# Performance work log

Hardware: AMD Instinct MI355X
Metric: run time of the kernel (lower is better)

The kernel has to match this reference:

```python
import jax, jax.numpy as jnp
import numpy as np

N = 50000
E = 600000
D_IN, D_HID, D_OUT = 128, 128, 64


def gcn_conv(x, edge_index, W, b):
    """PyG GCNConv: add self-loops, symmetric deg^{-1/2} normalization,
    linear transform, scatter-add aggregation, bias."""
    n = x.shape[0]
    loop = jnp.arange(n, dtype=edge_index.dtype)
    src = jnp.concatenate([edge_index[0], loop])
    dst = jnp.concatenate([edge_index[1], loop])
    h = x @ W  # [N, out]
    deg = jax.ops.segment_sum(jnp.ones_like(dst, dtype=h.dtype), dst, num_segments=n)
    dinv = jnp.where(deg > 0, jax.lax.rsqrt(jnp.maximum(deg, 1e-12)), 0.0)
    norm = dinv[src] * dinv[dst]  # [E+N]
    msg = h[src] * norm[:, None]  # gather + scale
    out = jax.ops.segment_sum(msg, dst, num_segments=n)  # scatter-add
    return out + b


def setup_inputs() -> dict:
    key = jax.random.key(0)
    k1, k2, k3, k4 = jax.random.split(key, 4)
    x = jax.random.normal(k1, (N, D_IN), dtype=jnp.float32)
    edge_index = jax.random.randint(k2, (2, E), 0, N, dtype=jnp.int64)
    s1 = (1.0 / np.sqrt(D_IN)).astype(np.float32) if False else np.float32(1.0 / np.sqrt(D_IN))
    s2 = np.float32(1.0 / np.sqrt(D_HID))
    W1 = jax.random.normal(k3, (D_IN, D_HID), dtype=jnp.float32) * s1
    b1 = jnp.zeros((D_HID,), dtype=jnp.float32)
    W2 = jax.random.normal(k4, (D_HID, D_OUT), dtype=jnp.float32) * s2
    b2 = jnp.zeros((D_OUT,), dtype=jnp.float32)
    return {"x": x, "edge_index": edge_index, "W1": W1, "b1": b1, "W2": W2, "b2": b2}


def reference(x, edge_index, W1, b1, W2, b2):
    # eval mode: dropout p = 0
    h = jax.nn.relu(gcn_conv(x, edge_index, W1, b1))
    return gcn_conv(h, edge_index, W2, b2)
```

## Files before the change

### kernel.cpp

```cpp
#include <hip/hip_runtime.h>
#include <hip/hip_fp16.h>
#include <stdint.h>

#define DIN 128
#define DHID 128
#define DOUT2 64

typedef __attribute__((ext_vector_type(8))) short short8v;
typedef __attribute__((ext_vector_type(4))) float f32x4;

__device__ __forceinline__ unsigned short f2bf(float f) {
    unsigned u = __float_as_uint(f);
    u += 0x7fffu + ((u >> 16) & 1u);
    return (unsigned short)(u >> 16);
}
__device__ __forceinline__ float bf2f(unsigned short b) {
    return __uint_as_float(((unsigned)b) << 16);
}
__device__ __forceinline__ float bflo(unsigned v) { return __uint_as_float(v << 16); }
__device__ __forceinline__ float bfhi(unsigned v) { return __uint_as_float(v & 0xffff0000u); }
__device__ __forceinline__ unsigned short f2h(float f) {
    return __half_as_ushort(__float2half_rn(f));
}
__device__ __forceinline__ float h2f(unsigned bits) {
    return __half2float(__ushort_as_half((unsigned short)bits));
}

__global__ void detect_i64_kernel(const unsigned* ei, int* flag) {
    int t = threadIdx.x;
    unsigned hi = ei[2 * t + 1];
    unsigned long long vote = __ballot(hi == 0u);
    if (t == 0) *flag = (vote == ~0ull) ? 1 : 0;
}

__global__ void deg_count_kernel(const int* ei32, const long long* ei64, const int* flag,
                                 unsigned* deg, int E) {
    int e = blockIdx.x * blockDim.x + threadIdx.x;
    if (e >= E) return;
    int mode = *flag;
    int d = mode ? (int)ei64[(size_t)E + e] : ei32[(size_t)E + e];
    atomicAdd(&deg[d], 1u);
}

template <int DO, typename AT>
__global__ __launch_bounds__(256) void gemm_mfma_kernel(const AT* __restrict__ A,
                                                        const float* __restrict__ W,
                                                        unsigned short* __restrict__ out,
                                                        int M) {
    constexpr int NT = DO / 16;
    __shared__ unsigned short As[64 * 136];
    __shared__ unsigned short Wt[DO * 136];
    const int tid = threadIdx.x;
    const int row0 = blockIdx.x * 64;

    for (int idx = tid; idx < 128 * (DO / 4); idx += 256) {
        int k = idx / (DO / 4);
        int n4 = (idx % (DO / 4)) * 4;
        float4 w = ((const float4*)W)[idx];
        Wt[(n4 + 0) * 136 + k] = f2bf(w.x);
        Wt[(n4 + 1) * 136 + k] = f2bf(w.y);
        Wt[(n4 + 2) * 136 + k] = f2bf(w.z);
        Wt[(n4 + 3) * 136 + k] = f2bf(w.w);
    }
    if constexpr (sizeof(AT) == 4) {
        for (int idx = tid; idx < 64 * 32; idx += 256) {
            int r = idx >> 5, c4 = idx & 31;
            int row = row0 + r;
            ushort4 o = {0, 0, 0, 0};
            if (row < M) {
                float4 v = ((const float4*)A)[(size_t)row * 32 + c4];
                o.x = f2bf(v.x);
                o.y = f2bf(v.y);
                o.z = f2bf(v.z);
                o.w = f2bf(v.w);
            }
            *(ushort4*)&As[r * 136 + c4 * 4] = o;
        }
    } else {
        for (int idx = tid; idx < 64 * 16; idx += 256) {
            int r = idx >> 4, c8 = idx & 15;
            int row = row0 + r;
            uint4 v = {0u, 0u, 0u, 0u};
            if (row < M) v = ((const uint4*)A)[(size_t)row * 16 + c8];
            *(uint4*)&As[r * 136 + c8 * 8] = v;
        }
    }
    __syncthreads();

    const int wid = tid >> 6, lane = tid & 63;
    const int r16 = lane & 15, g = lane >> 4;
    f32x4 acc[NT];
#pragma unroll
    for (int n = 0; n < NT; n++) acc[n] = (f32x4){0.f, 0.f, 0.f, 0.f};

    const unsigned short* a_base = &As[(wid * 16 + r16) * 136 + g * 8];
    const unsigned short* b_base = &Wt[r16 * 136 + g * 8];
#pragma unroll
    for (int kk = 0; kk < 4; kk++) {
        short8v a = *(const short8v*)(a_base + kk * 32);
#pragma unroll
        for (int n = 0; n < NT; n++) {
            short8v b = *(const short8v*)(b_base + n * 16 * 136 + kk * 32);
            acc[n] = __builtin_amdgcn_mfma_f32_16x16x32_bf16(a, b, acc[n], 0, 0, 0);
        }
    }

    const int rbase = row0 + wid * 16 + g * 4;
#pragma unroll
    for (int n = 0; n < NT; n++) {
#pragma unroll
        for (int q = 0; q < 4; q++) {
            int row = rbase + q;
            if (row < M) out[(size_t)row * DO + n * 16 + r16] = f2bf(acc[n][q]);
        }
    }
}

__global__ __launch_bounds__(256) void scan_blocksum_kernel(const unsigned* deg, int* bsum,
                                                            float* dinv, int N) {
    __shared__ int s[256];
    int t = threadIdx.x;
    int base = blockIdx.x * 1024 + t * 4;
    int sum = 0;
    if (base + 3 < N) {
        int4 v = *(const int4*)((const int*)deg + base);
        sum = v.x + v.y + v.z + v.w;
        float4 dv;
        dv.x = rsqrtf((float)(v.x + 1));
        dv.y = rsqrtf((float)(v.y + 1));
        dv.z = rsqrtf((float)(v.z + 1));
        dv.w = rsqrtf((float)(v.w + 1));
        *(float4*)(dinv + base) = dv;
    } else {
        for (int j = 0; j < 4; j++)
            if (base + j < N) {
                int d = (int)deg[base + j];
                sum += d;
                dinv[base + j] = rsqrtf((float)(d + 1));
            }
    }
    s[t] = sum;
    __syncthreads();
    for (int off = 128; off > 0; off >>= 1) {
        if (t < off) s[t] += s[t + off];
        __syncthreads();
    }
    if (t == 0) bsum[blockIdx.x] = s[0];
}

__global__ __launch_bounds__(256) void scan_bsum_kernel(int* bsum, int* row_ptr, int nb, int N) {
    __shared__ int s[256];
    int t = threadIdx.x;
    int v = (t < nb) ? bsum[t] : 0;
    s[t] = v;
    __syncthreads();
    for (int off = 1; off < 256; off <<= 1) {
        int u = (t >= off) ? s[t - off] : 0;
        __syncthreads();
        s[t] += u;
        __syncthreads();
    }
    if (t < nb) bsum[t] = s[t] - v;
    if (t == 255) row_ptr[N] = s[255];
}

__global__ __launch_bounds__(256) void scan_write_kernel(const unsigned* deg, const int* bsum,
                                                         int* row_ptr, int* cursor, int N) {
    __shared__ int s[256];
    int t = threadIdx.x;
    int base = blockIdx.x * 1024 + t * 4;
    int d[4];
    int sum = 0;
#pragma unroll
    for (int j = 0; j < 4; j++) {
        int idx = base + j;
        d[j] = (idx < N) ? (int)deg[idx] : 0;
        sum += d[j];
    }
    s[t] = sum;
    __syncthreads();
    for (int off = 1; off < 256; off <<= 1) {
        int u = (t >= off) ? s[t - off] : 0;
        __syncthreads();
        s[t] += u;
        __syncthreads();
    }
    int run = bsum[blockIdx.x] + s[t] - sum;
#pragma unroll
    for (int j = 0; j < 4; j++) {
        int idx = base + j;
        if (idx < N) {
            row_ptr[idx] = run;
            cursor[idx] = run;
            run += d[j];
        }
    }
}

__global__ void scatter_pack32_kernel(const int* ei32, const long long* ei64, const int* flag,
                                      const float* dinv, int* cursor, unsigned* csr, int E) {
    int e = blockIdx.x * blockDim.x + threadIdx.x;
    if (e >= E) return;
    int mode = *flag;
    int s, d;
    if (mode) {
        s = (int)ei64[e];
        d = (int)ei64[(size_t)E + e];
    } else {
        s = ei32[e];
        d = ei32[(size_t)E + e];
    }
    int pos = atomicAdd(&cursor[d], 1);
    csr[pos] = (unsigned)s | ((unsigned)f2h(dinv[s]) << 16);
}

__global__ void scatter_pack64_kernel(const int* ei32, const long long* ei64, const int* flag,
                                      const float* dinv, int* cursor, unsigned long long* csr,
                                      int E) {
    int e = blockIdx.x * blockDim.x + threadIdx.x;
    if (e >= E) return;
    int mode = *flag;
    int s, d;
    if (mode) {
        s = (int)ei64[e];
        d = (int)ei64[(size_t)E + e];
    } else {
        s = ei32[e];
        d = ei32[(size_t)E + e];
    }
    int pos = atomicAdd(&cursor[d], 1);
    csr[pos] = (unsigned long long)(unsigned)s |
               ((unsigned long long)__float_as_uint(dinv[s]) << 32);
}

__device__ __forceinline__ void unpack(unsigned p, int& s, float& w) {
    s = (int)(p & 0xffffu);
    w = h2f(p >> 16);
}
__device__ __forceinline__ void unpack(unsigned long long p, int& s, float& w) {
    s = (int)(unsigned)(p & 0xffffffffu);
    w = __uint_as_float((unsigned)(p >> 32));
}

template <int D, bool RELU, typename OT, typename CT>
__global__ __launch_bounds__(256) void agg_kernel(const unsigned short* __restrict__ h,
                                                  const CT* __restrict__ csr,
                                                  const int* __restrict__ row_ptr,
                                                  const float* __restrict__ dinv,
                                                  const float* __restrict__ bias,
                                                  OT* __restrict__ out, int N) {
    const int wid = threadIdx.x >> 6;
    const int lane = threadIdx.x & 63;
    const int i = blockIdx.x * 4 + wid;
    if (i >= N) return;
    const float di = dinv[i];
    const int start = row_ptr[i], end = row_ptr[i + 1];

    if constexpr (D == 128) {
        const unsigned* hu = (const unsigned*)h;
        unsigned sv = hu[(size_t)i * 64 + lane];
        float a0 = di * bflo(sv), b0 = di * bfhi(sv);
        float a1 = 0.f, b1 = 0.f;
        int j = start;
        for (; j + 4 <= end; j += 4) {
            CT p0 = csr[j], p1 = csr[j + 1], p2 = csr[j + 2], p3 = csr[j + 3];
            int s0, s1, s2, s3;
            float w0, w1, w2, w3;
            unpack(p0, s0, w0);
            unpack(p1, s1, w1);
            unpack(p2, s2, w2);
            unpack(p3, s3, w3);
            unsigned v0 = hu[(size_t)s0 * 64 + lane];
            unsigned v1 = hu[(size_t)s1 * 64 + lane];
            unsigned v2 = hu[(size_t)s2 * 64 + lane];
            unsigned v3 = hu[(size_t)s3 * 64 + lane];
            a0 = fmaf(w0, bflo(v0), a0);
            b0 = fmaf(w0, bfhi(v0), b0);
            a1 = fmaf(w1, bflo(v1), a1);
            b1 = fmaf(w1, bfhi(v1), b1);
            a0 = fmaf(w2, bflo(v2), a0);
            b0 = fmaf(w2, bfhi(v2), b0);
            a1 = fmaf(w3, bflo(v3), a1);
            b1 = fmaf(w3, bfhi(v3), b1);
        }
        for (; j < end; ++j) {
            int s0;
            float w0;
            unpack(csr[j], s0, w0);
            unsigned v0 = hu[(size_t)s0 * 64 + lane];
            a0 = fmaf(w0, bflo(v0), a0);
            b0 = fmaf(w0, bfhi(v0), b0);
        }
        float2 bv = ((const float2*)bias)[lane];
        float rx = di * (a0 + a1) + bv.x;
        float ry = di * (b0 + b1) + bv.y;
        if (RELU) {
            rx = fmaxf(rx, 0.f);
            ry = fmaxf(ry, 0.f);
        }
        if constexpr (sizeof(OT) == 2) {
            unsigned pv = (unsigned)f2bf(rx) | ((unsigned)f2bf(ry) << 16);
            ((unsigned*)out)[(size_t)i * 64 + lane] = pv;
        } else {
            ((float2*)out)[(size_t)i * 64 + lane] = make_float2(rx, ry);
        }
    } else {
        float a0 = di * bf2f(h[(size_t)i * 64 + lane]);
        float a1 = 0.f;
        int j = start;
        for (; j + 4 <= end; j += 4) {
            CT p0 = csr[j], p1 = csr[j + 1], p2 = csr[j + 2], p3 = csr[j + 3];
            int s0, s1, s2, s3;
            float w0, w1, w2, w3;
            unpack(p0, s0, w0);
            unpack(p1, s1, w1);
            unpack(p2, s2, w2);
            unpack(p3, s3, w3);
            float v0 = bf2f(h[(size_t)s0 * 64 + lane]);
            float v1 = bf2f(h[(size_t)s1 * 64 + lane]);
            float v2 = bf2f(h[(size_t)s2 * 64 + lane]);
            float v3 = bf2f(h[(size_t)s3 * 64 + lane]);
            a0 = fmaf(w0, v0, a0);
            a1 = fmaf(w1, v1, a1);
            a0 = fmaf(w2, v2, a0);
            a1 = fmaf(w3, v3, a1);
        }
        for (; j < end; ++j) {
            int s0;
            float w0;
            unpack(csr[j], s0, w0);
            a0 = fmaf(w0, bf2f(h[(size_t)s0 * 64 + lane]), a0);
        }
        float r = di * (a0 + a1) + bias[lane];
        if (RELU) r = fmaxf(r, 0.f);
        if constexpr (sizeof(OT) == 2) {
            out[(size_t)i * 64 + lane] = (OT)f2bf(r);
        } else {
            out[(size_t)i * 64 + lane] = r;
        }
    }
}

extern "C" void kernel_launch(void* const* d_in, const int* in_sizes, int n_in,
                              void* d_out, int out_size, void* d_ws, size_t ws_size,
                              hipStream_t stream) {
    const float* x  = (const float*)d_in[0];
    const void*  ei = d_in[1];
    const float* W1 = (const float*)d_in[2];
    const float* b1 = (const float*)d_in[3];
    const float* W2 = (const float*)d_in[4];
    const float* b2 = (const float*)d_in[5];
    float* out = (float*)d_out;

    const int N = in_sizes[0] / DIN;
    const int E = in_sizes[1] / 2;

    char* ws = (char*)d_ws;
    size_t off = 0;
    auto alloc = [&](size_t bytes) -> void* {
        void* p = ws + off;
        off += (bytes + 255) & ~(size_t)255;
        return p;
    };
    unsigned*       deg  = (unsigned*)alloc((size_t)N * 4);
    float*          dinv = (float*)alloc((size_t)N * 4);
    int*            rowp = (int*)alloc((size_t)(N + 1) * 4);
    int*            curs = (int*)alloc((size_t)N * 4);
    int*            flag = (int*)alloc(256);
    int*            bsum = (int*)alloc(1024 * 4);
    void*           csr  = alloc((size_t)E * 8);
    unsigned short* h1   = (unsigned short*)alloc((size_t)N * DHID * 2);
    unsigned short* o1   = (unsigned short*)alloc((size_t)N * DHID * 2);
    unsigned short* h2   = h1;

    const int nb = (N + 1023) / 1024;
    const int gemmBlocks = (N + 63) / 64;
    const int degBlocks = (E + 255) / 256;

    hipMemsetAsync(deg, 0, (size_t)N * 4, stream);
    detect_i64_kernel<<<1, 64, 0, stream>>>((const unsigned*)ei, flag);
    deg_count_kernel<<<degBlocks, 256, 0, stream>>>((const int*)ei, (const long long*)ei, flag,
                                                    deg, E);
    gemm_mfma_kernel<DHID, float><<<gemmBlocks, 256, 0, stream>>>(x, W1, h1, N);
    scan_blocksum_kernel<<<nb, 256, 0, stream>>>(deg, bsum, dinv, N);
    scan_bsum_kernel<<<1, 256, 0, stream>>>(bsum, rowp, nb, N);
    scan_write_kernel<<<nb, 256, 0, stream>>>(deg, bsum, rowp, curs, N);

    if (N <= 65535) {
        unsigned* csr32 = (unsigned*)csr;
        scatter_pack32_kernel<<<degBlocks, 256, 0, stream>>>(
            (const int*)ei, (const long long*)ei, flag, dinv, curs, csr32, E);
        agg_kernel<DHID, true, unsigned short, unsigned><<<(N + 3) / 4, 256, 0, stream>>>(
            h1, csr32, rowp, dinv, b1, o1, N);
        gemm_mfma_kernel<DOUT2, unsigned short><<<gemmBlocks, 256, 0, stream>>>(o1, W2, h2, N);
        agg_kernel<DOUT2, false, float, unsigned><<<(N + 3) / 4, 256, 0, stream>>>(
            h2, csr32, rowp, dinv, b2, out, N);
    } else {
        unsigned long long* csr64 = (unsigned long long*)csr;
        scatter_pack64_kernel<<<degBlocks, 256, 0, stream>>>(
            (const int*)ei, (const long long*)ei, flag, dinv, curs, csr64, E);
        agg_kernel<DHID, true, unsigned short, unsigned long long><<<(N + 3) / 4, 256, 0,
                                                                     stream>>>(h1, csr64, rowp,
                                                                               dinv, b1, o1, N);
        gemm_mfma_kernel<DOUT2, unsigned short><<<gemmBlocks, 256, 0, stream>>>(o1, W2, h2, N);
        agg_kernel<DOUT2, false, float, unsigned long long><<<(N + 3) / 4, 256, 0, stream>>>(
            h2, csr64, rowp, dinv, b2, out, N);
    }
}
```

Before: 243.3 us.

## Pre-transpose weights once, fuse index-width detection into kernels, unroll aggregation by 8

A new prep kernel converts W1 and W2 to transposed bf16 once and also does the degree count with inline index-width detection. This removes the separate detect kernel, the flag memory read, and the per-block weight conversion in every GEMM block. The GEMM now reads B fragments straight from global or L2 instead of padded shared memory. The aggregation loops are unrolled to 8 edges with four accumulator pairs to keep more gathers in flight. The cost is that B loads now go through global memory rather than LDS, and register pressure in the aggregation kernel goes up.

```diff
diff --git a/kernel.cpp b/kernel.cpp
--- a/kernel.cpp
+++ b/kernel.cpp
@@ -26,42 +26,45 @@
     return __half2float(__ushort_as_half((unsigned short)bits));
 }
 
-__global__ void detect_i64_kernel(const unsigned* ei, int* flag) {
-    int t = threadIdx.x;
-    unsigned hi = ei[2 * t + 1];
-    unsigned long long vote = __ballot(hi == 0u);
-    if (t == 0) *flag = (vote == ~0ull) ? 1 : 0;
-}
-
-__global__ void deg_count_kernel(const int* ei32, const long long* ei64, const int* flag,
-                                 unsigned* deg, int E) {
-    int e = blockIdx.x * blockDim.x + threadIdx.x;
-    if (e >= E) return;
-    int mode = *flag;
-    int d = mode ? (int)ei64[(size_t)E + e] : ei32[(size_t)E + e];
-    atomicAdd(&deg[d], 1u);
+__device__ __forceinline__ int detect_mode(const unsigned* ei) {
+    int lane = threadIdx.x & 63;
+    unsigned hi = ei[2 * lane + 1];
+    return (__ballot(hi == 0u) == ~0ull) ? 1 : 0;
+}
+
+__global__ void prep_kernel(const float* __restrict__ W1, const float* __restrict__ W2,
+                            unsigned short* __restrict__ wt1, unsigned short* __restrict__ wt2,
+                            const int* ei32, const long long* ei64, unsigned* deg, int E) {
+    if (blockIdx.x == 0) {
+        for (int idx = threadIdx.x; idx < 128 * 128; idx += 256) {
+            int n = idx & 127, k = idx >> 7;
+            wt1[n * 128 + k] = f2bf(W1[idx]);
+        }
+    } else if (blockIdx.x == 1) {
+        for (int idx = threadIdx.x; idx < 128 * 64; idx += 256) {
+            int n = idx & 63, k = idx >> 6;
+            wt2[n * 128 + k] = f2bf(W2[idx]);
+        }
+    } else {
+        int mode = detect_mode((const unsigned*)ei32);
+        int e = (blockIdx.x - 2) * 256 + threadIdx.x;
+        if (e < E) {
+            int d = mode ? (int)ei64[(size_t)E + e] : ei32[(size_t)E + e];
+            atomicAdd(&deg[d], 1u);
+        }
+    }
 }
 
 template <int DO, typename AT>
 __global__ __launch_bounds__(256) void gemm_mfma_kernel(const AT* __restrict__ A,
-                                                        const float* __restrict__ W,
+                                                        const unsigned short* __restrict__ Wt,
                                                         unsigned short* __restrict__ out,
                                                         int M) {
     constexpr int NT = DO / 16;
     __shared__ unsigned short As[64 * 136];
-    __shared__ unsigned short Wt[DO * 136];
     const int tid = threadIdx.x;
     const int row0 = blockIdx.x * 64;
 
-    for (int idx = tid; idx < 128 * (DO / 4); idx += 256) {
-        int k = idx / (DO / 4);
-        int n4 = (idx % (DO / 4)) * 4;
-        float4 w = ((const float4*)W)[idx];
-        Wt[(n4 + 0) * 136 + k] = f2bf(w.x);
-        Wt[(n4 + 1) * 136 + k] = f2bf(w.y);
-        Wt[(n4 + 2) * 136 + k] = f2bf(w.z);
-        Wt[(n4 + 3) * 136 + k] = f2bf(w.w);
-    }
     if constexpr (sizeof(AT) == 4) {
         for (int idx = tid; idx < 64 * 32; idx += 256) {
             int r = idx >> 5, c4 = idx & 31;
@@ -94,13 +97,13 @@
     for (int n = 0; n < NT; n++) acc[n] = (f32x4){0.f, 0.f, 0.f, 0.f};
 
     const unsigned short* a_base = &As[(wid * 16 + r16) * 136 + g * 8];
-    const unsigned short* b_base = &Wt[r16 * 136 + g * 8];
+    const unsigned short* b_base = Wt + r16 * 128 + g * 8;
 #pragma unroll
     for (int kk = 0; kk < 4; kk++) {
         short8v a = *(const short8v*)(a_base + kk * 32);
 #pragma unroll
         for (int n = 0; n < NT; n++) {
-            short8v b = *(const short8v*)(b_base + n * 16 * 136 + kk * 32);
+            short8v b = *(const short8v*)(b_base + n * 16 * 128 + kk * 32);
             acc[n] = __builtin_amdgcn_mfma_f32_16x16x32_bf16(a, b, acc[n], 0, 0, 0);
         }
     }
@@ -197,11 +200,11 @@
     }
 }
 
-__global__ void scatter_pack32_kernel(const int* ei32, const long long* ei64, const int* flag,
-                                      const float* dinv, int* cursor, unsigned* csr, int E) {
+__global__ void scatter_pack32_kernel(const int* ei32, const long long* ei64, const float* dinv,
+                                      int* cursor, unsigned* csr, int E) {
+    int mode = detect_mode((const unsigned*)ei32);
     int e = blockIdx.x * blockDim.x + threadIdx.x;
     if (e >= E) return;
-    int mode = *flag;
     int s, d;
     if (mode) {
         s = (int)ei64[e];
@@ -214,12 +217,11 @@
     csr[pos] = (unsigned)s | ((unsigned)f2h(dinv[s]) << 16);
 }
 
-__global__ void scatter_pack64_kernel(const int* ei32, const long long* ei64, const int* flag,
-                                      const float* dinv, int* cursor, unsigned long long* csr,
-                                      int E) {
+__global__ void scatter_pack64_kernel(const int* ei32, const long long* ei64, const float* dinv,
+                                      int* cursor, unsigned long long* csr, int E) {
+    int mode = detect_mode((const unsigned*)ei32);
     int e = blockIdx.x * blockDim.x + threadIdx.x;
     if (e >= E) return;
-    int mode = *flag;
     int s, d;
     if (mode) {
         s = (int)ei64[e];
@@ -260,28 +262,32 @@
         const unsigned* hu = (const unsigned*)h;
         unsigned sv = hu[(size_t)i * 64 + lane];
         float a0 = di * bflo(sv), b0 = di * bfhi(sv);
-        float a1 = 0.f, b1 = 0.f;
+        float a1 = 0.f, b1 = 0.f, a2 = 0.f, b2 = 0.f, a3 = 0.f, b3 = 0.f;
         int j = start;
-        for (; j + 4 <= end; j += 4) {
-            CT p0 = csr[j], p1 = csr[j + 1], p2 = csr[j + 2], p3 = csr[j + 3];
-            int s0, s1, s2, s3;
-            float w0, w1, w2, w3;
-            unpack(p0, s0, w0);
-            unpack(p1, s1, w1);
-            unpack(p2, s2, w2);
-            unpack(p3, s3, w3);
-            unsigned v0 = hu[(size_t)s0 * 64 + lane];
-            unsigned v1 = hu[(size_t)s1 * 64 + lane];
-            unsigned v2 = hu[(size_t)s2 * 64 + lane];
-            unsigned v3 = hu[(size_t)s3 * 64 + lane];
-            a0 = fmaf(w0, bflo(v0), a0);
-            b0 = fmaf(w0, bfhi(v0), b0);
-            a1 = fmaf(w1, bflo(v1), a1);
-            b1 = fmaf(w1, bfhi(v1), b1);
-            a0 = fmaf(w2, bflo(v2), a0);
-            b0 = fmaf(w2, bfhi(v2), b0);
-            a1 = fmaf(w3, bflo(v3), a1);
-            b1 = fmaf(w3, bfhi(v3), b1);
+        for (; j + 8 <= end; j += 8) {
+            int s[8];
+            float w[8];
+            unsigned v[8];
+#pragma unroll
+            for (int u = 0; u < 8; u++) unpack(csr[j + u], s[u], w[u]);
+#pragma unroll
+            for (int u = 0; u < 8; u++) v[u] = hu[(size_t)s[u] * 64 + lane];
+            a0 = fmaf(w[0], bflo(v[0]), a0);
+            b0 = fmaf(w[0], bfhi(v[0]), b0);
+            a1 = fmaf(w[1], bflo(v[1]), a1);
+            b1 = fmaf(w[1], bfhi(v[1]), b1);
+            a2 = fmaf(w[2], bflo(v[2]), a2);
+            b2 = fmaf(w[2], bfhi(v[2]), b2);
+            a3 = fmaf(w[3], bflo(v[3]), a3);
+            b3 = fmaf(w[3], bfhi(v[3]), b3);
+            a0 = fmaf(w[4], bflo(v[4]), a0);
+            b0 = fmaf(w[4], bfhi(v[4]), b0);
+            a1 = fmaf(w[5], bflo(v[5]), a1);
+            b1 = fmaf(w[5], bfhi(v[5]), b1);
+            a2 = fmaf(w[6], bflo(v[6]), a2);
+            b2 = fmaf(w[6], bfhi(v[6]), b2);
+            a3 = fmaf(w[7], bflo(v[7]), a3);
+            b3 = fmaf(w[7], bfhi(v[7]), b3);
         }
         for (; j < end; ++j) {
             int s0;
@@ -292,8 +298,8 @@
             b0 = fmaf(w0, bfhi(v0), b0);
         }
         float2 bv = ((const float2*)bias)[lane];
-        float rx = di * (a0 + a1) + bv.x;
-        float ry = di * (b0 + b1) + bv.y;
+        float rx = di * ((a0 + a1) + (a2 + a3)) + bv.x;
+        float ry = di * ((b0 + b1) + (b2 + b3)) + bv.y;
         if (RELU) {
             rx = fmaxf(rx, 0.f);
             ry = fmaxf(ry, 0.f);
@@ -306,24 +312,24 @@
         }
     } else {
         float a0 = di * bf2f(h[(size_t)i * 64 + lane]);
-        float a1 = 0.f;
+        float a1 = 0.f, a2 = 0.f, a3 = 0.f;
         int j = start;
-        for (; j + 4 <= end; j += 4) {
-            CT p0 = csr[j], p1 = csr[j + 1], p2 = csr[j + 2], p3 = csr[j + 3];
-            int s0, s1, s2, s3;
-            float w0, w1, w2, w3;
-            unpack(p0, s0, w0);
-            unpack(p1, s1, w1);
-            unpack(p2, s2, w2);
-            unpack(p3, s3, w3);
-            float v0 = bf2f(h[(size_t)s0 * 64 + lane]);
-            float v1 = bf2f(h[(size_t)s1 * 64 + lane]);
-            float v2 = bf2f(h[(size_t)s2 * 64 + lane]);
-            float v3 = bf2f(h[(size_t)s3 * 64 + lane]);
-            a0 = fmaf(w0, v0, a0);
-            a1 = fmaf(w1, v1, a1);
-            a0 = fmaf(w2, v2, a0);
-            a1 = fmaf(w3, v3, a1);
+        for (; j + 8 <= end; j += 8) {
+            int s[8];
+            float w[8];
+            float v[8];
+#pragma unroll
+            for (int u = 0; u < 8; u++) unpack(csr[j + u], s[u], w[u]);
+#pragma unroll
+            for (int u = 0; u < 8; u++) v[u] = bf2f(h[(size_t)s[u] * 64 + lane]);
+            a0 = fmaf(w[0], v[0], a0);
+            a1 = fmaf(w[1], v[1], a1);
+            a2 = fmaf(w[2], v[2], a2);
+            a3 = fmaf(w[3], v[3], a3);
+            a0 = fmaf(w[4], v[4], a0);
+            a1 = fmaf(w[5], v[5], a1);
+            a2 = fmaf(w[6], v[6], a2);
+            a3 = fmaf(w[7], v[7], a3);
         }
         for (; j < end; ++j) {
             int s0;
@@ -331,7 +337,7 @@
             unpack(csr[j], s0, w0);
             a0 = fmaf(w0, bf2f(h[(size_t)s0 * 64 + lane]), a0);
         }
-        float r = di * (a0 + a1) + bias[lane];
+        float r = di * ((a0 + a1) + (a2 + a3)) + bias[lane];
         if (RELU) r = fmaxf(r, 0.f);
         if constexpr (sizeof(OT) == 2) {
             out[(size_t)i * 64 + lane] = (OT)f2bf(r);
@@ -366,8 +372,9 @@
     float*          dinv = (float*)alloc((size_t)N * 4);
     int*            rowp = (int*)alloc((size_t)(N + 1) * 4);
     int*            curs = (int*)alloc((size_t)N * 4);
-    int*            flag = (int*)alloc(256);
     int*            bsum = (int*)alloc(1024 * 4);
+    unsigned short* wt1  = (unsigned short*)alloc(128 * 128 * 2);
+    unsigned short* wt2  = (unsigned short*)alloc(128 * 64 * 2);
     void*           csr  = alloc((size_t)E * 8);
     unsigned short* h1   = (unsigned short*)alloc((size_t)N * DHID * 2);
     unsigned short* o1   = (unsigned short*)alloc((size_t)N * DHID * 2);
@@ -378,31 +385,32 @@
     const int degBlocks = (E + 255) / 256;
 
     hipMemsetAsync(deg, 0, (size_t)N * 4, stream);
-    detect_i64_kernel<<<1, 64, 0, stream>>>((const unsigned*)ei, flag);
-    deg_count_kernel<<<degBlocks, 256, 0, stream>>>((const int*)ei, (const long long*)ei, flag,
-                                                    deg, E);
-    gemm_mfma_kernel<DHID, float><<<gemmBlocks, 256, 0, stream>>>(x, W1, h1, N);
+    prep_kernel<<<2 + degBlocks, 256, 0, stream>>>(W1, W2, wt1, wt2, (const int*)ei,
+                                                   (const long long*)ei, deg, E);
+    gemm_mfma_kernel<DHID, float><<<gemmBlocks, 256, 0, stream>>>(x, wt1, h1, N);
     scan_blocksum_kernel<<<nb, 256, 0, stream>>>(deg, bsum, dinv, N);
     scan_bsum_kernel<<<1, 256, 0, stream>>>(bsum, rowp, nb, N);
     scan_write_kernel<<<nb, 256, 0, stream>>>(deg, bsum, rowp, curs, N);
 
     if (N <= 65535) {
         unsigned* csr32 = (unsigned*)csr;
-        scatter_pack32_kernel<<<degBlocks, 256, 0, stream>>>(
-            (const int*)ei, (const long long*)ei, flag, dinv, curs, csr32, E);
+        scatter_pack32_kernel<<<degBlocks, 256, 0, stream>>>((const int*)ei,
+                                                             (const long long*)ei, dinv, curs,
+                                                             csr32, E);
         agg_kernel<DHID, true, unsigned short, unsigned><<<(N + 3) / 4, 256, 0, stream>>>(
             h1, csr32, rowp, dinv, b1, o1, N);
-        gemm_mfma_kernel<DOUT2, unsigned short><<<gemmBlocks, 256, 0, stream>>>(o1, W2, h2, N);
+        gemm_mfma_kernel<DOUT2, unsigned short><<<gemmBlocks, 256, 0, stream>>>(o1, wt2, h2, N);
         agg_kernel<DOUT2, false, float, unsigned><<<(N + 3) / 4, 256, 0, stream>>>(
             h2, csr32, rowp, dinv, b2, out, N);
     } else {
         unsigned long long* csr64 = (unsigned long long*)csr;
-        scatter_pack64_kernel<<<degBlocks, 256, 0, stream>>>(
-            (const int*)ei, (const long long*)ei, flag, dinv, curs, csr64, E);
+        scatter_pack64_kernel<<<degBlocks, 256, 0, stream>>>((const int*)ei,
+                                                             (const long long*)ei, dinv, curs,
+                                                             csr64, E);
         agg_kernel<DHID, true, unsigned short, unsigned long long><<<(N + 3) / 4, 256, 0,
                                                                      stream>>>(h1, csr64, rowp,
                                                                                dinv, b1, o1, N);
-        gemm_mfma_kernel<DOUT2, unsigned short><<<gemmBlocks, 256, 0, stream>>>(o1, W2, h2, N);
+        gemm_mfma_kernel<DOUT2, unsigned short><<<gemmBlocks, 256, 0, stream>>>(o1, wt2, h2, N);
         agg_kernel<DOUT2, false, float, unsigned long long><<<(N + 3) / 4, 256, 0, stream>>>(
             h2, csr64, rowp, dinv, b2, out, N);
     }
```

New measurement: 247.4 us. Within noise of the previous version (+1.7%).
